# Performance work log

Measured on AMD Instinct MI355X. Metric: run time of the kernel, lower is better.

Reference implementation:

```python
import jax, jax.numpy as jnp
import numpy as np

F_DIM = 32          # phi_feature_dim
P = 128             # preselection_ap (spatial H=W)
NU = 4              # num_users
N1 = NU - 1         # n_cat1 == n_cat2
N3 = (NU - 1) ** 2  # n_cat3


def setup_inputs() -> dict:
    key = jax.random.key(0)
    k1, k2, k3, k4, k5 = jax.random.split(key, 5)
    B, CIN = 32, 8
    phi_input = jax.random.normal(k1, (B, CIN, P, P), dtype=jnp.float32)
    W1 = jax.random.normal(k2, (4 * F_DIM, CIN), dtype=jnp.float32) * 0.1
    b1 = jax.random.normal(k3, (4 * F_DIM,), dtype=jnp.float32) * 0.1
    W3 = jax.random.normal(k4, (4 * F_DIM, 4 * F_DIM), dtype=jnp.float32) * 0.1
    b3 = jax.random.normal(k5, (4 * F_DIM,), dtype=jnp.float32) * 0.1
    ex = jnp.ones((P, P), dtype=jnp.float32) - jnp.eye(P, dtype=jnp.float32)
    return {"phi_input": phi_input, "W1": W1, "b1": b1, "W3": W3, "b3": b3, "ex": ex}


def _conv1x1(x, W, b):
    # 1x1 conv == channel matmul: [b,c,h,w] x [o,c] -> [b,o,h,w]
    return jnp.einsum('bchw,oc->bohw', x, W) + b[None, :, None, None]


def _postprocess(r, ex):
    f = F_DIM
    c0 = r[:, :f]
    c1 = jnp.einsum('ph,bchw->bcpw', ex, r[:, f:2 * f]) / N1
    c2 = jnp.einsum('bchw,wq->bchq', r[:, 2 * f:3 * f], ex) / N1
    c3 = jnp.einsum('ph,bchw,wq->bcpq', ex, r[:, 3 * f:4 * f], ex) / N3
    return jnp.concatenate((c0, c1, c2, c3), axis=1)


def reference(phi_input, W1, b1, W3, b3, ex):
    r = jax.nn.relu(_conv1x1(phi_input, W1, b1))
    r = _postprocess(r, ex)
    r = jax.nn.relu(_conv1x1(r, W3, b3))
    r = _postprocess(r, ex)
    return r
```

## Files before the change

kernel.cpp:

```cpp
#include <hip/hip_runtime.h>
#include <stdint.h>

#define BATCH 32
#define CIN   8
#define NCH   128
#define PP    128
#define NSTRIP 8
#define KSTRIP 16

typedef __attribute__((ext_vector_type(8))) short    bf16x8;
typedef __attribute__((ext_vector_type(4))) float    f32x4;

__device__ __forceinline__ float bf2f(unsigned short u) {
    union { unsigned int i; float f; } x; x.i = ((unsigned int)u) << 16; return x.f;
}
__device__ __forceinline__ unsigned short f2bf(float f) {
    union { float f; unsigned int i; } x; x.f = f;
    unsigned int r = x.i + 0x7fffu + ((x.i >> 16) & 1u);
    return (unsigned short)(r >> 16);
}
__device__ __forceinline__ unsigned int pk2(float a, float b) {
    return (unsigned int)f2bf(a) | ((unsigned int)f2bf(b) << 16);
}

#define SWZB(row, cb) (((row) << 8) + ((cb) ^ (((row) & 7) << 4)))

__global__ __launch_bounds__(512, 4) void k1_sums(const float* __restrict__ phi,
        const float* __restrict__ W1, const float* __restrict__ b1,
        float* __restrict__ RS1t, float* __restrict__ CS1p) {
    __shared__ float cs_f[128 * 132];
    __shared__ unsigned short phi_b[2][1024];
    int bx = blockIdx.x;
    int b = bx >> 3, strip = bx & 7;
    int p0 = strip * 16;
    int tid = threadIdx.x;
    int wv = tid >> 6, l = tid & 63, lr = l & 15, lg = l >> 4;
    int c0 = wv * 16 + lg * 4;

    bf16x8 w1fr = {0, 0, 0, 0, 0, 0, 0, 0};
    if (lg == 0) {
        int cc = wv * 16 + lr;
        float4 wa = *(const float4*)(W1 + cc * 8);
        float4 wb = *(const float4*)(W1 + cc * 8 + 4);
        w1fr[0] = (short)f2bf(wa.x); w1fr[1] = (short)f2bf(wa.y);
        w1fr[2] = (short)f2bf(wa.z); w1fr[3] = (short)f2bf(wa.w);
        w1fr[4] = (short)f2bf(wb.x); w1fr[5] = (short)f2bf(wb.y);
        w1fr[6] = (short)f2bf(wb.z); w1fr[7] = (short)f2bf(wb.w);
    }
    f32x4 binit = {b1[c0], b1[c0 + 1], b1[c0 + 2], b1[c0 + 3]};
    if (tid < 128) {
        bf16x8 pv;
        #pragma unroll
        for (int ci = 0; ci < 8; ++ci)
            pv[ci] = (short)f2bf(phi[((size_t)(b * CIN + ci) * PP + p0) * PP + tid]);
        *(bf16x8*)(phi_b[0] + tid * 8) = pv;
    }
    __syncthreads();

    f32x4 cs_acc[8];
    #pragma unroll
    for (int i = 0; i < 8; ++i) { f32x4 z = {0.f, 0.f, 0.f, 0.f}; cs_acc[i] = z; }

    int cur = 0;
    for (int r = 0; r < 16; ++r) {
        int p = p0 + r;
        float pfv[8];
        if (r < 15 && tid < 128) {
            #pragma unroll
            for (int ci = 0; ci < 8; ++ci)
                pfv[ci] = phi[((size_t)(b * CIN + ci) * PP + p + 1) * PP + tid];
        }
        const unsigned short* pb = phi_b[cur];
        f32x4 rs4 = {0.f, 0.f, 0.f, 0.f};
        #pragma unroll
        for (int pt = 0; pt < 8; ++pt) {
            int pix = pt * 16 + lr;
            bf16x8 bfr1 = {0, 0, 0, 0, 0, 0, 0, 0};
            if (lg == 0) bfr1 = *(const bf16x8*)(pb + pix * 8);
            f32x4 a = __builtin_amdgcn_mfma_f32_16x16x32_bf16(w1fr, bfr1, binit, 0, 0, 0);
            f32x4 v = {fmaxf(a.x, 0.f), fmaxf(a.y, 0.f), fmaxf(a.z, 0.f), fmaxf(a.w, 0.f)};
            cs_acc[pt] += v;
            rs4 += v;
        }
        #pragma unroll
        for (int m = 1; m < 16; m <<= 1) {
            rs4.x += __shfl_xor(rs4.x, m);
            rs4.y += __shfl_xor(rs4.y, m);
            rs4.z += __shfl_xor(rs4.z, m);
            rs4.w += __shfl_xor(rs4.w, m);
        }
        if (lr == 0)
            *(f32x4*)(RS1t + ((size_t)b * PP + p) * NCH + c0) = rs4;
        if (r < 15 && tid < 128) {
            bf16x8 pv;
            #pragma unroll
            for (int ci = 0; ci < 8; ++ci) pv[ci] = (short)f2bf(pfv[ci]);
            *(bf16x8*)(phi_b[cur ^ 1] + tid * 8) = pv;
        }
        __syncthreads();
        cur ^= 1;
    }
    #pragma unroll
    for (int pt = 0; pt < 8; ++pt) {
        f32x4 v = cs_acc[pt];
        int q = pt * 16 + lr;
        cs_f[(c0 + 0) * 132 + q] = v.x;
        cs_f[(c0 + 1) * 132 + q] = v.y;
        cs_f[(c0 + 2) * 132 + q] = v.z;
        cs_f[(c0 + 3) * 132 + q] = v.w;
    }
    __syncthreads();
    float* dstp = CS1p + (size_t)(b * NSTRIP + strip) * NCH * PP;
    for (int k = tid; k < 16384; k += 512) {
        int cc = k >> 7, q = k & 127;
        dstp[k] = cs_f[cc * 132 + q];
    }
}

__global__ __launch_bounds__(256) void k1b_planes(const float* __restrict__ W3,
        const float* __restrict__ b3, const float* __restrict__ RS1t,
        const float* __restrict__ CS1p, float* __restrict__ Ap,
        float* __restrict__ Bqt, unsigned short* __restrict__ W3bf) {
    int bx = blockIdx.x;
    int b = bx >> 2, og = bx & 3;
    int tid = threadIdx.x;
    __shared__ float cs_g[64][132];
    __shared__ float rs_g[64][132];
    __shared__ float s1_96[32];
    for (int k = tid; k < 64 * 128; k += 256) {
        int r = k >> 7, q = k & 127;
        int ch_c = (r < 32) ? (32 + r) : (64 + r);
        float s = 0.f;
        #pragma unroll
        for (int s8 = 0; s8 < NSTRIP; ++s8)
            s += CS1p[((size_t)(b * NSTRIP + s8) * NCH + ch_c) * PP + q];
        cs_g[r][q] = s;
    }
    for (int k = tid; k < 64 * 128; k += 256) {
        int p = k >> 6, r = k & 63;
        rs_g[r][p] = RS1t[((size_t)b * PP + p) * NCH + 64 + r];
    }
    __syncthreads();
    if (tid < 32) {
        float s = 0.f;
        for (int q = 0; q < 128; ++q) s += cs_g[32 + tid][q];
        s1_96[tid] = s;
    }
    int o = og * 32 + (tid >> 3), qh = tid & 7;
    {
        float wa[64];
        #pragma unroll
        for (int r = 0; r < 64; ++r)
            wa[r] = (r < 32) ? W3[o * NCH + 32 + r] * (1.f / 3.f)
                             : -W3[o * NCH + 64 + r] * (1.f / 9.f);
        #pragma unroll
        for (int j = 0; j < 4; ++j) {
            int q = qh * 16 + j * 4;
            float4 a = {0.f, 0.f, 0.f, 0.f};
            #pragma unroll
            for (int r = 0; r < 64; ++r) {
                float4 cv = *(const float4*)&cs_g[r][q];
                a.x = fmaf(wa[r], cv.x, a.x);
                a.y = fmaf(wa[r], cv.y, a.y);
                a.z = fmaf(wa[r], cv.z, a.z);
                a.w = fmaf(wa[r], cv.w, a.w);
            }
            *(float4*)&Ap[((size_t)b * NCH + o) * PP + q] = a;
        }
    }
    __syncthreads();
    float cc = b3[o];
    #pragma unroll
    for (int r = 0; r < 32; ++r)
        cc = fmaf(W3[o * NCH + 96 + r] * (1.f / 9.f), s1_96[r], cc);
    {
        float wb[64];
        #pragma unroll
        for (int r = 0; r < 64; ++r)
            wb[r] = (r < 32) ? W3[o * NCH + 64 + r] * (1.f / 3.f)
                             : -W3[o * NCH + 64 + r] * (1.f / 9.f);
        #pragma unroll
        for (int j = 0; j < 4; ++j) {
            int p4 = qh * 16 + j * 4;
            float4 a = {0.f, 0.f, 0.f, 0.f};
            #pragma unroll
            for (int r = 0; r < 64; ++r) {
                float4 rv = *(const float4*)&rs_g[r][p4];
                a.x = fmaf(wb[r], rv.x, a.x);
                a.y = fmaf(wb[r], rv.y, a.y);
                a.z = fmaf(wb[r], rv.z, a.z);
                a.w = fmaf(wb[r], rv.w, a.w);
            }
            Bqt[((size_t)b * PP + p4 + 0) * NCH + o] = a.x + cc;
            Bqt[((size_t)b * PP + p4 + 1) * NCH + o] = a.y + cc;
            Bqt[((size_t)b * PP + p4 + 2) * NCH + o] = a.z + cc;
            Bqt[((size_t)b * PP + p4 + 3) * NCH + o] = a.w + cc;
        }
    }
    if (bx == 0) {
        for (int i = 0; i < 16; ++i) {
            int k = tid + i * 256;
            float4 w = *(const float4*)(W3 + k * 4);
            int c0 = (k * 4) & 127;
            float sc = (c0 < 32) ? 1.f : ((c0 < 96) ? (-1.f / 3.f) : (1.f / 9.f));
            unsigned int lo = pk2(w.x * sc, w.y * sc);
            unsigned int hi = pk2(w.z * sc, w.w * sc);
            uint2 u = {lo, hi};
            *(uint2*)(W3bf + k * 4) = u;
        }
    }
}

__global__ __launch_bounds__(512) void k2a_sums(const float* __restrict__ phi,
        const float* __restrict__ W1, const float* __restrict__ b1,
        const unsigned short* __restrict__ W3bf,
        const float* __restrict__ Ap, const float* __restrict__ Bqt,
        float* __restrict__ RSvT, float* __restrict__ CSp) {
    int bx = blockIdx.x;
    int b = bx >> 4, strip = bx & 15;
    int p0 = strip * 8;
    __shared__ unsigned short w3_l[16384];
    __shared__ unsigned short t_l[16384];
    __shared__ unsigned short phi_b[2][1024];
    __shared__ float BC_l[2][128];
    __shared__ float rs_part[8][64];
    int tid = threadIdx.x;
    int wv = tid >> 6, l = tid & 63, lr = l & 15, lg = l >> 4;
    int q0 = wv * 16 + lg * 4;
    int c0 = q0;

    #pragma unroll
    for (int i = 0; i < 4; ++i) {
        int k = tid + i * 512;
        int o = k >> 4, cb = (k & 15) * 16;
        bf16x8 v = *(const bf16x8*)(W3bf + k * 8);
        *(bf16x8*)((char*)w3_l + SWZB(o, cb)) = v;
    }
    bf16x8 w1fr = {0, 0, 0, 0, 0, 0, 0, 0};
    if (lg == 0) {
        int cc = wv * 16 + lr;
        float4 wa = *(const float4*)(W1 + cc * 8);
        float4 wb = *(const float4*)(W1 + cc * 8 + 4);
        w1fr[0] = (short)f2bf(wa.x); w1fr[1] = (short)f2bf(wa.y);
        w1fr[2] = (short)f2bf(wa.z); w1fr[3] = (short)f2bf(wa.w);
        w1fr[4] = (short)f2bf(wb.x); w1fr[5] = (short)f2bf(wb.y);
        w1fr[6] = (short)f2bf(wb.z); w1fr[7] = (short)f2bf(wb.w);
    }
    f32x4 binit = {b1[c0], b1[c0 + 1], b1[c0 + 2], b1[c0 + 3]};
    f32x4 apr[6];
    #pragma unroll
    for (int nt = 2; nt < 8; ++nt)
        apr[nt - 2] = *(const f32x4*)(Ap + ((size_t)(b * NCH + nt * 16 + lr)) * PP + q0);
    if (tid < 128) {
        bf16x8 pv;
        #pragma unroll
        for (int ci = 0; ci < 8; ++ci)
            pv[ci] = (short)f2bf(phi[((size_t)(b * CIN + ci) * PP + p0) * PP + tid]);
        *(bf16x8*)(phi_b[0] + tid * 8) = pv;
        BC_l[0][tid] = Bqt[((size_t)b * PP + p0) * NCH + tid];
    }
    __syncthreads();

    f32x4 cs1a = {0.f,0.f,0.f,0.f}, cs1b = {0.f,0.f,0.f,0.f};
    f32x4 cs3a = {0.f,0.f,0.f,0.f}, cs3b = {0.f,0.f,0.f,0.f};

    for (int r = 0; r < 8; ++r) {
        int cur = r & 1, nxt = cur ^ 1;
        int p = p0 + r;
        float pfv[8]; float bcn = 0.f;
        if (r < 7 && tid < 128) {
            #pragma unroll
            for (int ci = 0; ci < 8; ++ci)
                pfv[ci] = phi[((size_t)(b * CIN + ci) * PP + p + 1) * PP + tid];
            bcn = Bqt[((size_t)b * PP + p + 1) * NCH + tid];
        }
        const unsigned short* pb = phi_b[cur];
        #pragma unroll
        for (int pt = 0; pt < 8; ++pt) {
            int pix = pt * 16 + lr;
            bf16x8 bfr1 = {0, 0, 0, 0, 0, 0, 0, 0};
            if (lg == 0) bfr1 = *(const bf16x8*)(pb + pix * 8);
            f32x4 a = __builtin_amdgcn_mfma_f32_16x16x32_bf16(w1fr, bfr1, binit, 0, 0, 0);
            uint2 u;
            u.x = pk2(fmaxf(a.x, 0.f), fmaxf(a.y, 0.f));
            u.y = pk2(fmaxf(a.z, 0.f), fmaxf(a.w, 0.f));
            *(uint2*)((char*)t_l + SWZB(pix, c0 * 2)) = u;
        }
        __syncthreads();
        bf16x8 afr[4];
        #pragma unroll
        for (int ks = 0; ks < 4; ++ks)
            afr[ks] = *(const bf16x8*)((char*)t_l + SWZB(wv * 16 + lr, ks * 64 + lg * 16));
        #pragma unroll
        for (int nt = 2; nt < 8; ++nt) {
            int o = nt * 16 + lr;
            bf16x8 bfr[4];
            #pragma unroll
            for (int ks = 0; ks < 4; ++ks)
                bfr[ks] = *(const bf16x8*)((char*)w3_l + SWZB(o, ks * 64 + lg * 16));
            f32x4 acc = apr[nt - 2] + BC_l[cur][o];
            #pragma unroll
            for (int ks = 0; ks < 4; ++ks)
                acc = __builtin_amdgcn_mfma_f32_16x16x32_bf16(afr[ks], bfr[ks], acc, 0, 0, 0);
            f32x4 v = {fmaxf(acc.x, 0.f), fmaxf(acc.y, 0.f), fmaxf(acc.z, 0.f), fmaxf(acc.w, 0.f)};
            if (nt == 2) cs1a += v;
            else if (nt == 3) cs1b += v;
            else if (nt == 6) cs3a += v;
            else if (nt == 7) cs3b += v;
            if (nt >= 4) {
                float rsv = v.x + v.y + v.z + v.w;
                rsv += __shfl_xor(rsv, 16);
                rsv += __shfl_xor(rsv, 32);
                if (lg == 0) rs_part[wv][(nt - 4) * 16 + lr] = rsv;
            }
        }
        if (r < 7 && tid < 128) {
            bf16x8 pv;
            #pragma unroll
            for (int ci = 0; ci < 8; ++ci) pv[ci] = (short)f2bf(pfv[ci]);
            *(bf16x8*)(phi_b[nxt] + tid * 8) = pv;
            BC_l[nxt][tid] = bcn;
        }
        __syncthreads();
        if (tid < 64) {
            float s = 0.f;
            #pragma unroll
            for (int w8 = 0; w8 < 8; ++w8) s += rs_part[w8][tid];
            RSvT[((size_t)(b * PP + p)) * 64 + tid] = s;
        }
    }
    {
        float* dst = CSp + ((size_t)(b * KSTRIP + strip)) * 64 * PP;
        *(f32x4*)(dst + (size_t)(lr)      * PP + q0) = cs1a;
        *(f32x4*)(dst + (size_t)(16 + lr) * PP + q0) = cs1b;
        *(f32x4*)(dst + (size_t)(32 + lr) * PP + q0) = cs3a;
        *(f32x4*)(dst + (size_t)(48 + lr) * PP + q0) = cs3b;
    }
}

__global__ __launch_bounds__(256) void k2s_reduce(const float* __restrict__ CSp,
        const float* __restrict__ RSvT, float* __restrict__ CSv,
        float* __restrict__ Sb) {
    int bx = blockIdx.x;
    int b = bx >> 3, grp = bx & 7;
    int tid = threadIdx.x;
    #pragma unroll
    for (int it = 0; it < 4; ++it) {
        int idx = grp * 1024 + it * 256 + tid;
        float s = 0.f;
        #pragma unroll
        for (int st = 0; st < KSTRIP; ++st)
            s += CSp[((size_t)(b * KSTRIP + st)) * 64 * PP + idx];
        CSv[(size_t)b * 64 * PP + idx] = s;
    }
    if (grp == 0 && tid < 32) {
        float s = 0.f;
        for (int p = 0; p < PP; ++p) s += RSvT[((size_t)(b * PP + p)) * 64 + 32 + tid];
        Sb[b * 32 + tid] = s;
    }
}

__global__ __launch_bounds__(512) void k2b_out(const float* __restrict__ phi,
        const float* __restrict__ W1, const float* __restrict__ b1,
        const unsigned short* __restrict__ W3bf,
        const float* __restrict__ Ap, const float* __restrict__ Bqt,
        const float* __restrict__ RSvT, const float* __restrict__ CSv,
        const float* __restrict__ Sb, float* __restrict__ out) {
    int bx = blockIdx.x;
    int b = bx >> 4, strip = bx & 15;
    int p0 = strip * 8;
    __shared__ unsigned short w3_l[16384];
    __shared__ unsigned short t_l[16384];
    __shared__ unsigned short phi_b[2][1024];
    __shared__ float BC_l[2][128];
    __shared__ float rs_row[2][64];
    int tid = threadIdx.x;
    int wv = tid >> 6, l = tid & 63, lr = l & 15, lg = l >> 4;
    int q0 = wv * 16 + lg * 4;
    int c0 = q0;

    #pragma unroll
    for (int i = 0; i < 4; ++i) {
        int k = tid + i * 512;
        int o = k >> 4, cb = (k & 15) * 16;
        bf16x8 v = *(const bf16x8*)(W3bf + k * 8);
        *(bf16x8*)((char*)w3_l + SWZB(o, cb)) = v;
    }
    bf16x8 w1fr = {0, 0, 0, 0, 0, 0, 0, 0};
    if (lg == 0) {
        int cc = wv * 16 + lr;
        float4 wa = *(const float4*)(W1 + cc * 8);
        float4 wb = *(const float4*)(W1 + cc * 8 + 4);
        w1fr[0] = (short)f2bf(wa.x); w1fr[1] = (short)f2bf(wa.y);
        w1fr[2] = (short)f2bf(wa.z); w1fr[3] = (short)f2bf(wa.w);
        w1fr[4] = (short)f2bf(wb.x); w1fr[5] = (short)f2bf(wb.y);
        w1fr[6] = (short)f2bf(wb.z); w1fr[7] = (short)f2bf(wb.w);
    }
    f32x4 binit = {b1[c0], b1[c0 + 1], b1[c0 + 2], b1[c0 + 3]};
    f32x4 apr[8];
    #pragma unroll
    for (int nt = 0; nt < 8; ++nt)
        apr[nt] = *(const f32x4*)(Ap + ((size_t)(b * NCH + nt * 16 + lr)) * PP + q0);
    f32x4 csr[4][2];
    float sjr[4];
    #pragma unroll
    for (int i = 0; i < 4; ++i) {
        int k = tid + i * 512;
        int o = k >> 4, j = k & 15;
        int g = o >> 5;
        f32x4 z = {0.f, 0.f, 0.f, 0.f};
        csr[i][0] = z; csr[i][1] = z; sjr[i] = 0.f;
        if (g == 1) {
            int jc = o - 32;
            csr[i][0] = *(const f32x4*)(CSv + ((size_t)b * 64 + jc) * PP + j * 8);
            csr[i][1] = *(const f32x4*)(CSv + ((size_t)b * 64 + jc) * PP + j * 8 + 4);
        } else if (g == 3) {
            int jc = 32 + (o - 96);
            csr[i][0] = *(const f32x4*)(CSv + ((size_t)b * 64 + jc) * PP + j * 8);
            csr[i][1] = *(const f32x4*)(CSv + ((size_t)b * 64 + jc) * PP + j * 8 + 4);
            sjr[i] = Sb[b * 32 + (o - 96)];
        }
    }
    if (tid < 128) {
        bf16x8 pv;
        #pragma unroll
        for (int ci = 0; ci < 8; ++ci)
            pv[ci] = (short)f2bf(phi[((size_t)(b * CIN + ci) * PP + p0) * PP + tid]);
        *(bf16x8*)(phi_b[0] + tid * 8) = pv;
        BC_l[0][tid] = Bqt[((size_t)b * PP + p0) * NCH + tid];
    } else if (tid < 192) {
        rs_row[0][tid - 128] = RSvT[((size_t)(b * PP + p0)) * 64 + tid - 128];
    }
    __syncthreads();

    for (int r = 0; r < 8; ++r) {
        int cur = r & 1, nxt = cur ^ 1;
        int p = p0 + r;
        float pfv[8]; float bcn = 0.f; float rsn = 0.f;
        if (r < 7) {
            if (tid < 128) {
                #pragma unroll
                for (int ci = 0; ci < 8; ++ci)
                    pfv[ci] = phi[((size_t)(b * CIN + ci) * PP + p + 1) * PP + tid];
                bcn = Bqt[((size_t)b * PP + p + 1) * NCH + tid];
            } else if (tid < 192) {
                rsn = RSvT[((size_t)(b * PP + p + 1)) * 64 + tid - 128];
            }
        }
        const unsigned short* pb = phi_b[cur];
        #pragma unroll
        for (int pt = 0; pt < 8; ++pt) {
            int pix = pt * 16 + lr;
            bf16x8 bfr1 = {0, 0, 0, 0, 0, 0, 0, 0};
            if (lg == 0) bfr1 = *(const bf16x8*)(pb + pix * 8);
            f32x4 a = __builtin_amdgcn_mfma_f32_16x16x32_bf16(w1fr, bfr1, binit, 0, 0, 0);
            uint2 u;
            u.x = pk2(fmaxf(a.x, 0.f), fmaxf(a.y, 0.f));
            u.y = pk2(fmaxf(a.z, 0.f), fmaxf(a.w, 0.f));
            *(uint2*)((char*)t_l + SWZB(pix, c0 * 2)) = u;
        }
        __syncthreads();
        bf16x8 afr[4];
        #pragma unroll
        for (int ks = 0; ks < 4; ++ks)
            afr[ks] = *(const bf16x8*)((char*)t_l + SWZB(wv * 16 + lr, ks * 64 + lg * 16));
        __syncthreads();
        #pragma unroll
        for (int nt = 0; nt < 8; ++nt) {
            int o = nt * 16 + lr;
            bf16x8 bfr[4];
            #pragma unroll
            for (int ks = 0; ks < 4; ++ks)
                bfr[ks] = *(const bf16x8*)((char*)w3_l + SWZB(o, ks * 64 + lg * 16));
            f32x4 acc = apr[nt] + BC_l[cur][o];
            #pragma unroll
            for (int ks = 0; ks < 4; ++ks)
                acc = __builtin_amdgcn_mfma_f32_16x16x32_bf16(afr[ks], bfr[ks], acc, 0, 0, 0);
            uint2 u;
            u.x = pk2(fmaxf(acc.x, 0.f), fmaxf(acc.y, 0.f));
            u.y = pk2(fmaxf(acc.z, 0.f), fmaxf(acc.w, 0.f));
            *(uint2*)((char*)t_l + SWZB(o, q0 * 2)) = u;
        }
        if (r < 7) {
            if (tid < 128) {
                bf16x8 pv;
                #pragma unroll
                for (int ci = 0; ci < 8; ++ci) pv[ci] = (short)f2bf(pfv[ci]);
                *(bf16x8*)(phi_b[nxt] + tid * 8) = pv;
                BC_l[nxt][tid] = bcn;
            } else if (tid < 192) {
                rs_row[nxt][tid - 128] = rsn;
            }
        }
        __syncthreads();
        #pragma unroll
        for (int i = 0; i < 4; ++i) {
            int k = tid + i * 512;
            int o = k >> 4, j = k & 15;
            int g = o >> 5;
            bf16x8 u = *(const bf16x8*)((char*)t_l + SWZB(o, j * 16));
            float rp = (g >= 2) ? rs_row[cur][o - 64] : 0.f;
            float o8[8];
            #pragma unroll
            for (int e = 0; e < 8; ++e) {
                float v = bf2f((unsigned short)u[e]);
                float cq = (e < 4) ? ((const float*)&csr[i][0])[e]
                                   : ((const float*)&csr[i][1])[e - 4];
                float rr;
                if (g == 0)      rr = v;
                else if (g == 1) rr = (cq - v) * (1.f / 3.f);
                else if (g == 2) rr = (rp - v) * (1.f / 3.f);
                else             rr = ((sjr[i] - rp) - cq + v) * (1.f / 9.f);
                o8[e] = rr;
            }
            f32x4 lo = {o8[0], o8[1], o8[2], o8[3]};
            f32x4 hi = {o8[4], o8[5], o8[6], o8[7]};
            float* dst = out + ((size_t)(b * NCH + o) * PP + p) * PP + j * 8;
            *(f32x4*)dst       = lo;
            *(f32x4*)(dst + 4) = hi;
        }
        __syncthreads();
    }
}

extern "C" void kernel_launch(void* const* d_in, const int* in_sizes, int n_in,
                              void* d_out, int out_size, void* d_ws, size_t ws_size,
                              hipStream_t stream) {
    (void)in_sizes; (void)n_in; (void)out_size; (void)ws_size;
    const float* phi = (const float*)d_in[0];
    const float* W1  = (const float*)d_in[1];
    const float* b1  = (const float*)d_in[2];
    const float* W3  = (const float*)d_in[3];
    const float* b3  = (const float*)d_in[4];
    float* out = (float*)d_out;

    char* ws = (char*)d_ws;
    size_t off = 0;
    float* RS1t = (float*)(ws + off); off += (size_t)BATCH * NCH * PP * 4;
    float* CS1p = (float*)(ws + off); off += (size_t)BATCH * NSTRIP * NCH * PP * 4;
    float* Ap   = (float*)(ws + off); off += (size_t)BATCH * NCH * PP * 4;
    float* Bqt  = (float*)(ws + off); off += (size_t)BATCH * NCH * PP * 4;
    unsigned short* W3bf = (unsigned short*)(ws + off); off += (size_t)NCH * NCH * 2;
    float* RSvT = (float*)(ws + off); off += (size_t)BATCH * PP * 64 * 4;
    float* CSp  = (float*)(ws + off); off += (size_t)BATCH * KSTRIP * 64 * PP * 4;
    float* CSv  = (float*)(ws + off); off += (size_t)BATCH * 64 * PP * 4;
    float* Sb   = (float*)(ws + off); off += (size_t)BATCH * 32 * 4;

    k1_sums<<<BATCH * NSTRIP, 512, 0, stream>>>(phi, W1, b1, RS1t, CS1p);
    k1b_planes<<<BATCH * 4, 256, 0, stream>>>(W3, b3, RS1t, CS1p, Ap, Bqt, W3bf);
    k2a_sums<<<BATCH * KSTRIP, 512, 0, stream>>>(phi, W1, b1, W3bf, Ap, Bqt, RSvT, CSp);
    k2s_reduce<<<BATCH * 8, 256, 0, stream>>>(CSp, RSvT, CSv, Sb);
    k2b_out<<<BATCH * KSTRIP, 512, 0, stream>>>(phi, W1, b1, W3bf, Ap, Bqt, RSvT, CSv, Sb, out);
}
```

Baseline: 186.7 us.

## Keep first-conv output in registers via wave shuffles instead of LDS staging

```diff
diff --git a/kernel.cpp b/kernel.cpp
--- a/kernel.cpp
+++ b/kernel.cpp
@@ -211,7 +211,7 @@
     }
 }
 
-__global__ __launch_bounds__(512) void k2a_sums(const float* __restrict__ phi,
+__global__ __launch_bounds__(512, 4) void k2a_sums(const float* __restrict__ phi,
         const float* __restrict__ W1, const float* __restrict__ b1,
         const unsigned short* __restrict__ W3bf,
         const float* __restrict__ Ap, const float* __restrict__ Bqt,
@@ -220,14 +220,12 @@
     int b = bx >> 4, strip = bx & 15;
     int p0 = strip * 8;
     __shared__ unsigned short w3_l[16384];
-    __shared__ unsigned short t_l[16384];
-    __shared__ unsigned short phi_b[2][1024];
+    __shared__ unsigned short phi_b[2][128 * 16];
     __shared__ float BC_l[2][128];
-    __shared__ float rs_part[8][64];
+    __shared__ float rs_part[2][8][64];
     int tid = threadIdx.x;
     int wv = tid >> 6, l = tid & 63, lr = l & 15, lg = l >> 4;
     int q0 = wv * 16 + lg * 4;
-    int c0 = q0;
 
     #pragma unroll
     for (int i = 0; i < 4; ++i) {
@@ -236,33 +234,45 @@
         bf16x8 v = *(const bf16x8*)(W3bf + k * 8);
         *(bf16x8*)((char*)w3_l + SWZB(o, cb)) = v;
     }
-    bf16x8 w1fr = {0, 0, 0, 0, 0, 0, 0, 0};
-    if (lg == 0) {
-        int cc = wv * 16 + lr;
-        float4 wa = *(const float4*)(W1 + cc * 8);
-        float4 wb = *(const float4*)(W1 + cc * 8 + 4);
-        w1fr[0] = (short)f2bf(wa.x); w1fr[1] = (short)f2bf(wa.y);
-        w1fr[2] = (short)f2bf(wa.z); w1fr[3] = (short)f2bf(wa.w);
-        w1fr[4] = (short)f2bf(wb.x); w1fr[5] = (short)f2bf(wb.y);
-        w1fr[6] = (short)f2bf(wb.z); w1fr[7] = (short)f2bf(wb.w);
-    }
-    f32x4 binit = {b1[c0], b1[c0 + 1], b1[c0 + 2], b1[c0 + 3]};
+    bf16x8 w1fr[8];
+    #pragma unroll
+    for (int nt = 0; nt < 8; ++nt) {
+        bf16x8 z = {0, 0, 0, 0, 0, 0, 0, 0};
+        w1fr[nt] = z;
+        int cch = nt * 16 + lr;
+        if (lg == 0) {
+            float4 wa = *(const float4*)(W1 + cch * 8);
+            float4 wb = *(const float4*)(W1 + cch * 8 + 4);
+            w1fr[nt][0] = (short)f2bf(wa.x); w1fr[nt][1] = (short)f2bf(wa.y);
+            w1fr[nt][2] = (short)f2bf(wa.z); w1fr[nt][3] = (short)f2bf(wa.w);
+            w1fr[nt][4] = (short)f2bf(wb.x); w1fr[nt][5] = (short)f2bf(wb.y);
+            w1fr[nt][6] = (short)f2bf(wb.z); w1fr[nt][7] = (short)f2bf(wb.w);
+        } else if (lg == 1) {
+            w1fr[nt][0] = (short)f2bf(b1[cch]);
+        }
+    }
     f32x4 apr[6];
     #pragma unroll
     for (int nt = 2; nt < 8; ++nt)
         apr[nt - 2] = *(const f32x4*)(Ap + ((size_t)(b * NCH + nt * 16 + lr)) * PP + q0);
     if (tid < 128) {
+        bf16x8 ones = {(short)0x3F80, 0, 0, 0, 0, 0, 0, 0};
+        *(bf16x8*)(phi_b[0] + tid * 16 + 8) = ones;
+        *(bf16x8*)(phi_b[1] + tid * 16 + 8) = ones;
         bf16x8 pv;
         #pragma unroll
         for (int ci = 0; ci < 8; ++ci)
             pv[ci] = (short)f2bf(phi[((size_t)(b * CIN + ci) * PP + p0) * PP + tid]);
-        *(bf16x8*)(phi_b[0] + tid * 8) = pv;
+        *(bf16x8*)(phi_b[0] + tid * 16) = pv;
         BC_l[0][tid] = Bqt[((size_t)b * PP + p0) * NCH + tid];
     }
     __syncthreads();
 
     f32x4 cs1a = {0.f,0.f,0.f,0.f}, cs1b = {0.f,0.f,0.f,0.f};
     f32x4 cs3a = {0.f,0.f,0.f,0.f}, cs3b = {0.f,0.f,0.f,0.f};
+    int srcA = ((lg & 1) * 2) * 16 + lr;
+    int srcB = srcA + 16;
+    bool hiHalf = (lg >= 2);
 
     for (int r = 0; r < 8; ++r) {
         int cur = r & 1, nxt = cur ^ 1;
@@ -274,34 +284,44 @@
                 pfv[ci] = phi[((size_t)(b * CIN + ci) * PP + p + 1) * PP + tid];
             bcn = Bqt[((size_t)b * PP + p + 1) * NCH + tid];
         }
-        const unsigned short* pb = phi_b[cur];
-        #pragma unroll
-        for (int pt = 0; pt < 8; ++pt) {
-            int pix = pt * 16 + lr;
-            bf16x8 bfr1 = {0, 0, 0, 0, 0, 0, 0, 0};
-            if (lg == 0) bfr1 = *(const bf16x8*)(pb + pix * 8);
-            f32x4 a = __builtin_amdgcn_mfma_f32_16x16x32_bf16(w1fr, bfr1, binit, 0, 0, 0);
-            uint2 u;
-            u.x = pk2(fmaxf(a.x, 0.f), fmaxf(a.y, 0.f));
-            u.y = pk2(fmaxf(a.z, 0.f), fmaxf(a.w, 0.f));
-            *(uint2*)((char*)t_l + SWZB(pix, c0 * 2)) = u;
-        }
-        __syncthreads();
+        bf16x8 bfr = {0, 0, 0, 0, 0, 0, 0, 0};
+        if (lg < 2) bfr = *(const bf16x8*)(phi_b[cur] + (wv * 16 + lr) * 16 + lg * 8);
+        f32x4 zero4 = {0.f, 0.f, 0.f, 0.f};
         bf16x8 afr[4];
         #pragma unroll
-        for (int ks = 0; ks < 4; ++ks)
-            afr[ks] = *(const bf16x8*)((char*)t_l + SWZB(wv * 16 + lr, ks * 64 + lg * 16));
+        for (int ks = 0; ks < 4; ++ks) {
+            f32x4 aa = __builtin_amdgcn_mfma_f32_16x16x32_bf16(w1fr[2 * ks],     bfr, zero4, 0, 0, 0);
+            f32x4 ab = __builtin_amdgcn_mfma_f32_16x16x32_bf16(w1fr[2 * ks + 1], bfr, zero4, 0, 0, 0);
+            unsigned int a0 = pk2(fmaxf(aa.x, 0.f), fmaxf(aa.y, 0.f));
+            unsigned int a1 = pk2(fmaxf(aa.z, 0.f), fmaxf(aa.w, 0.f));
+            unsigned int b0 = pk2(fmaxf(ab.x, 0.f), fmaxf(ab.y, 0.f));
+            unsigned int b1w = pk2(fmaxf(ab.z, 0.f), fmaxf(ab.w, 0.f));
+            unsigned int w0A = (unsigned int)__shfl((int)a0, srcA);
+            unsigned int w0B = (unsigned int)__shfl((int)b0, srcA);
+            unsigned int w1A = (unsigned int)__shfl((int)a1, srcA);
+            unsigned int w1B = (unsigned int)__shfl((int)b1w, srcA);
+            unsigned int w2A = (unsigned int)__shfl((int)a0, srcB);
+            unsigned int w2B = (unsigned int)__shfl((int)b0, srcB);
+            unsigned int w3A = (unsigned int)__shfl((int)a1, srcB);
+            unsigned int w3B = (unsigned int)__shfl((int)b1w, srcB);
+            uint4 u;
+            u.x = hiHalf ? w0B : w0A;
+            u.y = hiHalf ? w1B : w1A;
+            u.z = hiHalf ? w2B : w2A;
+            u.w = hiHalf ? w3B : w3A;
+            afr[ks] = *(bf16x8*)&u;
+        }
         #pragma unroll
         for (int nt = 2; nt < 8; ++nt) {
             int o = nt * 16 + lr;
-            bf16x8 bfr[4];
+            bf16x8 bfrw[4];
             #pragma unroll
             for (int ks = 0; ks < 4; ++ks)
-                bfr[ks] = *(const bf16x8*)((char*)w3_l + SWZB(o, ks * 64 + lg * 16));
+                bfrw[ks] = *(const bf16x8*)((char*)w3_l + SWZB(o, ks * 64 + lg * 16));
             f32x4 acc = apr[nt - 2] + BC_l[cur][o];
             #pragma unroll
             for (int ks = 0; ks < 4; ++ks)
-                acc = __builtin_amdgcn_mfma_f32_16x16x32_bf16(afr[ks], bfr[ks], acc, 0, 0, 0);
+                acc = __builtin_amdgcn_mfma_f32_16x16x32_bf16(afr[ks], bfrw[ks], acc, 0, 0, 0);
             f32x4 v = {fmaxf(acc.x, 0.f), fmaxf(acc.y, 0.f), fmaxf(acc.z, 0.f), fmaxf(acc.w, 0.f)};
             if (nt == 2) cs1a += v;
             else if (nt == 3) cs1b += v;
@@ -311,21 +331,21 @@
                 float rsv = v.x + v.y + v.z + v.w;
                 rsv += __shfl_xor(rsv, 16);
                 rsv += __shfl_xor(rsv, 32);
-                if (lg == 0) rs_part[wv][(nt - 4) * 16 + lr] = rsv;
+                if (lg == 0) rs_part[cur][wv][(nt - 4) * 16 + lr] = rsv;
             }
         }
         if (r < 7 && tid < 128) {
             bf16x8 pv;
             #pragma unroll
             for (int ci = 0; ci < 8; ++ci) pv[ci] = (short)f2bf(pfv[ci]);
-            *(bf16x8*)(phi_b[nxt] + tid * 8) = pv;
+            *(bf16x8*)(phi_b[nxt] + tid * 16) = pv;
             BC_l[nxt][tid] = bcn;
         }
         __syncthreads();
         if (tid < 64) {
             float s = 0.f;
             #pragma unroll
-            for (int w8 = 0; w8 < 8; ++w8) s += rs_part[w8][tid];
+            for (int w8 = 0; w8 < 8; ++w8) s += rs_part[cur][w8][tid];
             RSvT[((size_t)(b * PP + p)) * 64 + tid] = s;
         }
     }
```

After: 228.2 us. +22.3%, slower.
